# Optimization experiments

Hardware: AMD Instinct MI355X
Metric: run time of the kernel (lower is better)

Reference implementation:

```python
import jax, jax.numpy as jnp
import numpy as np

BATCH = 262144  # number of trajectories
# strictly increasing keyframe indices spanning frames 0..48 (n=13 knots, m=48 outputs)
KNOTS = np.array([0, 3, 7, 12, 16, 21, 25, 28, 32, 36, 41, 45, 48], dtype=np.int32)


def setup_inputs() -> dict:
    key = jax.random.key(0)
    index = jnp.asarray(KNOTS)
    value = jax.random.normal(key, (BATCH, KNOTS.shape[0], 2), dtype=jnp.float32)
    return {"index": index, "value": value}


def reference(index, value):
    # index is an integer knot vector -> treat as static (defines output length m).
    idx = np.asarray(index)
    m = int(idx[-1] - idx[0])
    # output sample points: start point excluded, end point included
    p = idx[0] + np.arange(1, m + 1)            # (m,)
    # segment i covers (idx[i], idx[i+1]]
    seg = np.searchsorted(idx, p, side="left") - 1  # (m,)

    pf = jnp.asarray(p, dtype=value.dtype)
    x0 = jnp.asarray(idx[seg], dtype=value.dtype)
    x1 = jnp.asarray(idx[seg + 1], dtype=value.dtype)
    t = ((pf - x0) / (x1 - x0))[:, None]        # (m, 1)

    start = value[..., seg, :]                  # (..., m, 2) gathered knot starts
    end = value[..., seg + 1, :]                # (..., m, 2) gathered knot ends
    return start + (end - start) * t
```

## Files before the change

kernel.cpp:

```cpp
#include <hip/hip_runtime.h>


#define BPB 64

__global__ __launch_bounds__(256)
void LinearInterpolation_20907900797406_kernel(
    const int* __restrict__ index,
    const float* __restrict__ value,
    float4* __restrict__ out4,
    int batch, int nk, int m) {
  __shared__ int   s_idx[32];
  __shared__ int   s_seg[64];
  __shared__ float s_t[64];
  __shared__ float s_val[BPB * 32];

  const int tid = threadIdx.x;
  if (tid < nk) s_idx[tid] = index[tid];
  __syncthreads();
  if (tid < m) {
    const int p = s_idx[0] + tid + 1;
    int cnt = 0;
    #pragma unroll 13
    for (int k = 0; k < nk; ++k) cnt += (s_idx[k] < p) ? 1 : 0;
    const int seg = cnt - 1;
    s_seg[tid] = seg;
    s_t[tid] = (float)(p - s_idx[seg]) / (float)(s_idx[seg + 1] - s_idx[seg]);
  }

  const int b0 = blockIdx.x * BPB;
  const int nb = min(BPB, batch - b0);
  const int nfl = nb * nk * 2;
  const int nf4 = nfl >> 2;
  const float4* src4 = (const float4*)(value + (long long)b0 * nk * 2);
  float4* s_val4 = (float4*)s_val;
  for (int i = tid; i < nf4; i += 256) s_val4[i] = src4[i];
  if (tid < (nfl & 3)) {
    s_val[(nf4 << 2) + tid] = value[(long long)b0 * nk * 2 + (nf4 << 2) + tid];
  }
  __syncthreads();

  const int half = m >> 1;
  const int npairs = nb * half;
  const long long outBase = (long long)b0 * half;
  const int row = nk * 2;
  for (int off = tid; off < npairs; off += 256) {
    const int bl = off / half;
    const int jp = off - bl * half;
    const float* vb = &s_val[bl * row];
    const int j0 = jp * 2;
    const int sa = s_seg[j0], sb = s_seg[j0 + 1];
    const float ta = s_t[j0], tb = s_t[j0 + 1];
    const float2 a0 = *(const float2*)&vb[2 * sa];
    const float2 e0 = *(const float2*)&vb[2 * sa + 2];
    const float2 a1 = *(const float2*)&vb[2 * sb];
    const float2 e1 = *(const float2*)&vb[2 * sb + 2];
    float4 o;
    o.x = a0.x + (e0.x - a0.x) * ta;
    o.y = a0.y + (e0.y - a0.y) * ta;
    o.z = a1.x + (e1.x - a1.x) * tb;
    o.w = a1.y + (e1.y - a1.y) * tb;
    out4[outBase + off] = o;
  }
}

extern "C" void kernel_launch(void* const* d_in, const int* in_sizes, int n_in,
                              void* d_out, int out_size, void* d_ws, size_t ws_size,
                              hipStream_t stream) {
  const int*   index = (const int*)d_in[0];
  const float* value = (const float*)d_in[1];
  float*       out   = (float*)d_out;

  const int nk    = in_sizes[0];
  const int batch = in_sizes[1] / (nk * 2);
  const int m     = out_size / (batch * 2);

  const int grid = (batch + BPB - 1) / BPB;
  LinearInterpolation_20907900797406_kernel<<<grid, 256, 0, stream>>>(
      index, value, (float4*)out, batch, nk, m);
}
```

Before: 127.6 us.

## Add specialized kernel with direct global-to-LDS loads and compile-time shapes

```diff
diff --git a/kernel.cpp b/kernel.cpp
--- a/kernel.cpp
+++ b/kernel.cpp
@@ -1,14 +1,105 @@
 #include <hip/hip_runtime.h>
+#include <stdint.h>
 
 
 #define BPB 64
 
-__global__ __launch_bounds__(256)
-void LinearInterpolation_20907900797406_kernel(
-    const int* __restrict__ index,
-    const float* __restrict__ value,
-    float4* __restrict__ out4,
-    int batch, int nk, int m) {
+typedef const __attribute__((address_space(1))) unsigned int* gas_t;
+typedef __attribute__((address_space(3))) unsigned int* las_t;
+
+static __device__ __forceinline__ void gload_lds16(const void* g, void* l) {
+  __builtin_amdgcn_global_load_lds((gas_t)g, (las_t)l, 16, 0, 0);
+}
+
+template <int NK, int M>
+__global__ __launch_bounds__(256) void lerp_fast(
+    const int* __restrict__ index, const float* __restrict__ value,
+    float4* __restrict__ out4) {
+  constexpr int HALF = M / 2;
+  constexpr int ROW  = NK * 2;
+  constexpr int NF4  = (BPB * ROW) / 4;
+  constexpr int ITER = (BPB * HALF) / 256;
+
+  __shared__ float4 s_val4[NF4];
+  __shared__ int2   s_seg[HALF];
+  __shared__ float2 s_t[HALF];
+
+  const int tid = threadIdx.x;
+  const int b0  = blockIdx.x * BPB;
+
+  {
+    const float4* src4 = (const float4*)(value + (size_t)b0 * ROW);
+    gload_lds16(src4 + tid, s_val4 + tid);
+    const int i = tid + 256;
+    if (i < NF4) gload_lds16(src4 + i, s_val4 + i);
+  }
+
+  if (tid < HALF) {
+    int kn[NK];
+#pragma unroll
+    for (int k = 0; k < NK; ++k) kn[k] = index[k];
+    const int p0 = kn[0] + 2 * tid + 1;
+    const int p1 = p0 + 1;
+    int c0 = 0, c1 = 0;
+#pragma unroll
+    for (int k = 0; k < NK; ++k) {
+      c0 += (kn[k] < p0) ? 1 : 0;
+      c1 += (kn[k] < p1) ? 1 : 0;
+    }
+    const int sa = c0 - 1, sb = c1 - 1;
+    s_seg[tid] = make_int2(sa, sb);
+    s_t[tid] = make_float2(
+        (float)(p0 - kn[sa]) / (float)(kn[sa + 1] - kn[sa]),
+        (float)(p1 - kn[sb]) / (float)(kn[sb + 1] - kn[sb]));
+  }
+  __syncthreads();
+
+  const float* s_val = (const float*)s_val4;
+  float4* __restrict__ dst = out4 + (size_t)b0 * HALF;
+#pragma unroll
+  for (int k = 0; k < ITER; ++k) {
+    const int off = tid + 256 * k;
+    const int bl = off / HALF;
+    const int jp = off - bl * HALF;
+    const int2   sg = s_seg[jp];
+    const float2 tt = s_t[jp];
+    const float* vb = s_val + bl * ROW;
+    const float2 a0 = *(const float2*)(vb + 2 * sg.x);
+    const float2 e0 = *(const float2*)(vb + 2 * sg.x + 2);
+    const float2 a1 = *(const float2*)(vb + 2 * sg.y);
+    const float2 e1 = *(const float2*)(vb + 2 * sg.y + 2);
+    float4 o;
+    o.x = fmaf(e0.x - a0.x, tt.x, a0.x);
+    o.y = fmaf(e0.y - a0.y, tt.x, a0.y);
+    o.z = fmaf(e1.x - a1.x, tt.y, a1.x);
+    o.w = fmaf(e1.y - a1.y, tt.y, a1.y);
+    dst[off] = o;
+  }
+  if constexpr ((BPB * HALF) % 256 != 0) {
+    const int off = tid + 256 * ITER;
+    if (off < BPB * HALF) {
+      const int bl = off / HALF;
+      const int jp = off - bl * HALF;
+      const int2   sg = s_seg[jp];
+      const float2 tt = s_t[jp];
+      const float* vb = s_val + bl * ROW;
+      const float2 a0 = *(const float2*)(vb + 2 * sg.x);
+      const float2 e0 = *(const float2*)(vb + 2 * sg.x + 2);
+      const float2 a1 = *(const float2*)(vb + 2 * sg.y);
+      const float2 e1 = *(const float2*)(vb + 2 * sg.y + 2);
+      float4 o;
+      o.x = fmaf(e0.x - a0.x, tt.x, a0.x);
+      o.y = fmaf(e0.y - a0.y, tt.x, a0.y);
+      o.z = fmaf(e1.x - a1.x, tt.y, a1.x);
+      o.w = fmaf(e1.y - a1.y, tt.y, a1.y);
+      dst[off] = o;
+    }
+  }
+}
+
+__global__ __launch_bounds__(256) void lerp_generic(
+    const int* __restrict__ index, const float* __restrict__ value,
+    float4* __restrict__ out4, int batch, int nk, int m, int bstart) {
   __shared__ int   s_idx[32];
   __shared__ int   s_seg[64];
   __shared__ float s_t[64];
@@ -20,14 +111,14 @@
   if (tid < m) {
     const int p = s_idx[0] + tid + 1;
     int cnt = 0;
-    #pragma unroll 13
+#pragma unroll 13
     for (int k = 0; k < nk; ++k) cnt += (s_idx[k] < p) ? 1 : 0;
     const int seg = cnt - 1;
     s_seg[tid] = seg;
     s_t[tid] = (float)(p - s_idx[seg]) / (float)(s_idx[seg + 1] - s_idx[seg]);
   }
 
-  const int b0 = blockIdx.x * BPB;
+  const int b0 = (bstart + blockIdx.x) * BPB;
   const int nb = min(BPB, batch - b0);
   const int nfl = nb * nk * 2;
   const int nf4 = nfl >> 2;
@@ -64,8 +155,8 @@
 }
 
 extern "C" void kernel_launch(void* const* d_in, const int* in_sizes, int n_in,
-                              void* d_out, int out_size, void* d_ws, size_t ws_size,
-                              hipStream_t stream) {
+                              void* d_out, int out_size, void* d_ws,
+                              size_t ws_size, hipStream_t stream) {
   const int*   index = (const int*)d_in[0];
   const float* value = (const float*)d_in[1];
   float*       out   = (float*)d_out;
@@ -74,7 +165,21 @@
   const int batch = in_sizes[1] / (nk * 2);
   const int m     = out_size / (batch * 2);
 
-  const int grid = (batch + BPB - 1) / BPB;
-  LinearInterpolation_20907900797406_kernel<<<grid, 256, 0, stream>>>(
-      index, value, (float4*)out, batch, nk, m);
+  const bool fast = (nk == 13) && (m == 48);
+  if (fast) {
+    const int fullBlocks = batch / BPB;
+    if (fullBlocks > 0) {
+      lerp_fast<13, 48><<<fullBlocks, 256, 0, stream>>>(index, value,
+                                                        (float4*)out);
+    }
+    const int rem = batch - fullBlocks * BPB;
+    if (rem > 0) {
+      lerp_generic<<<1, 256, 0, stream>>>(index, value, (float4*)out, batch,
+                                          nk, m, fullBlocks);
+    }
+  } else {
+    const int grid = (batch + BPB - 1) / BPB;
+    lerp_generic<<<grid, 256, 0, stream>>>(index, value, (float4*)out, batch,
+                                           nk, m, 0);
+  }
 }
```

After: 127.5 us. No clear change (-0.0%).
